# Kernel optimization log

Measured on AMD Instinct MI355X. Metric: run time of the kernel, lower is better.

## Reference

```python
import jax, jax.numpy as jnp
import numpy as np

N_WORDS, L_CHARS = 16384, 16
CHAR_SIZE, C_EMB = 128, 64
CONV_L, KERNEL, PAD = 256, 3, 2
VOCAB, D_EMB = 50000, 300
PAD_IDX = 1


def setup_inputs() -> dict:
    key = jax.random.key(0)
    k1, k2, k3, k4, k5, k6 = jax.random.split(key, 6)
    X = jax.random.randint(k1, (N_WORDS, L_CHARS), 0, CHAR_SIZE, dtype=jnp.int32)
    X_word = jax.random.randint(k2, (N_WORDS,), 0, VOCAB, dtype=jnp.int32)
    char_emb_w = jax.random.normal(k3, (CHAR_SIZE, C_EMB), dtype=jnp.float32)
    char_emb_w = char_emb_w.at[PAD_IDX].set(0.0)  # padding row zeroed, as in _init_char_embedding
    conv_w = jax.random.normal(k4, (CONV_L, C_EMB, KERNEL), dtype=jnp.float32) * 0.05
    conv_b = jax.random.normal(k5, (CONV_L,), dtype=jnp.float32) * 0.05
    word_emb_w = jax.random.normal(k6, (VOCAB, D_EMB), dtype=jnp.float32)
    return {"X": X, "X_word": X_word, "char_emb_w": char_emb_w,
            "conv_w": conv_w, "conv_b": conv_b, "word_emb_w": word_emb_w}


def reference(X, X_word, char_emb_w, conv_w, conv_b, word_emb_w):
    # char embedding lookup: [N, L, c_emb] -> NCH layout [N, c_emb, L]
    ce = char_emb_w[X].transpose(0, 2, 1)
    # Conv1d(c_emb -> conv_l, kernel=3, padding=2): out length L + 2*PAD - K + 1
    y = jax.lax.conv_general_dilated(
        ce, conv_w, window_strides=(1,), padding=[(PAD, PAD)],
        dimension_numbers=("NCH", "OIH", "NCH"))
    y = jax.nn.relu(y + conv_b[None, :, None])
    # MaxPool over the full time dimension -> [N, conv_l]
    char_feat = jnp.max(y, axis=2)
    # word embedding lookup: [N, d_emb]
    we = word_emb_w[X_word]
    return jnp.concatenate([char_feat, we], axis=1)
```

## Files before the change

### kernel.cpp

```cpp
#include <hip/hip_runtime.h>

#define N_WORDS   16384
#define L_CHARS   16
#define CHAR_SIZE 128
#define C_EMB     64
#define CONV_L    256
#define KERNEL_K  3
#define D_EMB     300
#define OUT_STRIDE (CONV_L + D_EMB)
#define CH_Q      64
#define SLICE_H   (CHAR_SIZE * KERNEL_K * CH_Q)

typedef _Float16 half8 __attribute__((ext_vector_type(8)));

static __device__ __forceinline__ half8 h8max(half8 a, half8 b) {
#if __has_builtin(__builtin_elementwise_max)
    return __builtin_elementwise_max(a, b);
#else
    half8 r;
    #pragma unroll
    for (int i = 0; i < 8; ++i) r[i] = a[i] > b[i] ? a[i] : b[i];
    return r;
#endif
}

__global__ void transpose_w(const float* __restrict__ w, float* __restrict__ Wt) {
    int tid = blockIdx.x * blockDim.x + threadIdx.x;
    if (tid >= CONV_L * C_EMB * KERNEL_K) return;
    int o = tid / (C_EMB * KERNEL_K);
    int r = tid - o * (C_EMB * KERNEL_K);
    int i = r / KERNEL_K;
    int k = r - i * KERNEL_K;
    Wt[i * (KERNEL_K * CONV_L) + k * CONV_L + o] = w[tid];
}

__global__ void build_table(const float* __restrict__ emb,
                            const float* __restrict__ Wt,
                            _Float16* __restrict__ Th) {
    int c = blockIdx.x / 3;
    int k = blockIdx.x % 3;
    int o = threadIdx.x;
    const float* erow = emb + c * C_EMB;
    float s = 0.f;
    #pragma unroll
    for (int i = 0; i < C_EMB; ++i)
        s += erow[i] * Wt[i * (KERNEL_K * CONV_L) + k * CONV_L + o];
    int q  = o >> 6;
    int oi = o & 63;
    Th[q * SLICE_H + c * (KERNEL_K * CH_Q) + k * CH_Q + oi] = (_Float16)s;
}

__global__ __launch_bounds__(256, 3)
void main_kernel(const int* __restrict__ X,
                 const int* __restrict__ Xw,
                 const _Float16* __restrict__ Th,
                 const float* __restrict__ conv_b,
                 const float* __restrict__ word_emb,
                 float* __restrict__ out,
                 int word_blocks) {
    __shared__ __align__(16) _Float16 Ts[SLICE_H];

    const int lane = threadIdx.x & 63;
    const int wv   = threadIdx.x >> 6;

    if ((int)blockIdx.x < word_blocks) {
        const int wavesTotal = word_blocks * 4;
        const int waveId = blockIdx.x * 4 + wv;
        for (int n = waveId; n < N_WORDS; n += wavesTotal) {
            int widx = Xw[n];
            const float4* src = (const float4*)(word_emb + (size_t)widx * D_EMB);
            float4* dst = (float4*)(out + (size_t)n * OUT_STRIDE + CONV_L);
            dst[lane] = src[lane];
            if (lane < (D_EMB / 4 - 64)) {
                dst[64 + lane] = src[64 + lane];
            }
        }
        return;
    }

    const int cb   = (int)blockIdx.x - word_blocks;
    const int q    = cb & 3;
    const int wgrp = cb >> 2;

    {
        const float4* src = (const float4*)(Th + q * SLICE_H);
        float4* dst = (float4*)Ts;
        #pragma unroll
        for (int i = 0; i < 12; ++i)
            dst[threadIdx.x + i * 256] = src[threadIdx.x + i * 256];
    }
    __syncthreads();

    const int g  = lane >> 3;
    const int l8 = lane & 7;

    float bias[8];
    {
        const float4* bp = (const float4*)(conv_b + q * CH_Q + l8 * 8);
        float4 b0 = bp[0], b1 = bp[1];
        bias[0]=b0.x; bias[1]=b0.y; bias[2]=b0.z; bias[3]=b0.w;
        bias[4]=b1.x; bias[5]=b1.y; bias[6]=b1.z; bias[7]=b1.w;
    }

    #pragma unroll
    for (int pass = 0; pass < 2; ++pass) {
        const int n = wgrp * 64 + pass * 32 + wv * 8 + g;

        const int4* xr = (const int4*)(X + n * L_CHARS);
        int4 q0 = xr[0], q1 = xr[1], q2 = xr[2], q3 = xr[3];
        int cs[16] = {q0.x, q0.y, q0.z, q0.w,
                      q1.x, q1.y, q1.z, q1.w,
                      q2.x, q2.y, q2.z, q2.w,
                      q3.x, q3.y, q3.z, q3.w};

        half8 a0 = (half8)(_Float16)0.f;
        half8 a1 = (half8)(_Float16)0.f;
        half8 m  = (half8)(_Float16)(-65504.f);

        #pragma unroll
        for (int j = 0; j < L_CHARS; ++j) {
            const _Float16* row = Ts + cs[j] * (KERNEL_K * CH_Q) + l8 * 8;
            half8 t0 = *(const half8*)(row);
            half8 t1 = *(const half8*)(row + CH_Q);
            half8 t2 = *(const half8*)(row + 2*CH_Q);
            half8 yj = a0 + t2;
            m  = h8max(m, yj);
            a0 = a1 + t1;
            a1 = t0;
        }
        m = h8max(m, a0);
        m = h8max(m, a1);

        float r[8];
        #pragma unroll
        for (int e = 0; e < 8; ++e)
            r[e] = fmaxf((float)m[e] + bias[e], 0.f);
        float4* dst = (float4*)(out + (size_t)n * OUT_STRIDE + q * CH_Q + l8 * 8);
        dst[0] = make_float4(r[0], r[1], r[2], r[3]);
        dst[1] = make_float4(r[4], r[5], r[6], r[7]);
    }
}

extern "C" void kernel_launch(void* const* d_in, const int* in_sizes, int n_in,
                              void* d_out, int out_size, void* d_ws, size_t ws_size,
                              hipStream_t stream) {
    const int*   X    = (const int*)d_in[0];
    const int*   Xw   = (const int*)d_in[1];
    const float* emb  = (const float*)d_in[2];
    const float* w    = (const float*)d_in[3];
    const float* b    = (const float*)d_in[4];
    const float* we   = (const float*)d_in[5];
    float* out = (float*)d_out;

    _Float16* Th = (_Float16*)d_ws;
    float*    Wt = (float*)((char*)d_ws + 4 * SLICE_H * sizeof(_Float16));

    transpose_w<<<(CONV_L * C_EMB * KERNEL_K + 255) / 256, 256, 0, stream>>>(w, Wt);
    build_table<<<CHAR_SIZE * KERNEL_K, 256, 0, stream>>>(emb, Wt, Th);

    const int WB = 256;
    const int CB = 1024;
    main_kernel<<<WB + CB, 256, 0, stream>>>(X, Xw, Th, b, we, out, WB);
}
```

Baseline: 134.4 us.

## Fuse weight transpose into table build and merge word gather into conv blocks

Drops the separate weight-transpose kernel: build_table now stages each 64-output chunk of conv weights in padded shared memory and computes all three taps per character block, which removes one launch. The main kernel shrinks from 1280 to 768 blocks. Each block processes one or two conv jobs in a grid-stride loop, and blocks 256 and up then gather 32 word-embedding rows each. Fewer launches and a grid that fits roughly one wave of residency are meant to cut launch and tail overhead. The cost is load imbalance, since some blocks do two conv jobs and others do a conv job plus word copies.

```diff
diff --git a/kernel.cpp b/kernel.cpp
--- a/kernel.cpp
+++ b/kernel.cpp
@@ -9,7 +9,8 @@
 #define D_EMB     300
 #define OUT_STRIDE (CONV_L + D_EMB)
 #define CH_Q      64
-#define SLICE_H   (CHAR_SIZE * KERNEL_K * CH_Q)
+#define T_ROWQ    (KERNEL_K * CH_Q)
+#define SLICE_H   (CHAR_SIZE * T_ROWQ)
 
 typedef _Float16 half8 __attribute__((ext_vector_type(8)));
 
@@ -24,30 +25,35 @@
 #endif
 }
 
-__global__ void transpose_w(const float* __restrict__ w, float* __restrict__ Wt) {
-    int tid = blockIdx.x * blockDim.x + threadIdx.x;
-    if (tid >= CONV_L * C_EMB * KERNEL_K) return;
-    int o = tid / (C_EMB * KERNEL_K);
-    int r = tid - o * (C_EMB * KERNEL_K);
-    int i = r / KERNEL_K;
-    int k = r - i * KERNEL_K;
-    Wt[i * (KERNEL_K * CONV_L) + k * CONV_L + o] = w[tid];
-}
+__global__ __launch_bounds__(256)
+void build_table(const float* __restrict__ emb,
+                 const float* __restrict__ w,
+                 _Float16* __restrict__ Th) {
+    __shared__ float wl[64 * 193];
+    const int c  = blockIdx.x;
+    const int t  = threadIdx.x;
+    const int kk = t >> 6;
+    const int ol = t & 63;
 
-__global__ void build_table(const float* __restrict__ emb,
-                            const float* __restrict__ Wt,
-                            _Float16* __restrict__ Th) {
-    int c = blockIdx.x / 3;
-    int k = blockIdx.x % 3;
-    int o = threadIdx.x;
-    const float* erow = emb + c * C_EMB;
-    float s = 0.f;
     #pragma unroll
-    for (int i = 0; i < C_EMB; ++i)
-        s += erow[i] * Wt[i * (KERNEL_K * CONV_L) + k * CONV_L + o];
-    int q  = o >> 6;
-    int oi = o & 63;
-    Th[q * SLICE_H + c * (KERNEL_K * CH_Q) + k * CH_Q + oi] = (_Float16)s;
+    for (int chunk = 0; chunk < 4; ++chunk) {
+        __syncthreads();
+        #pragma unroll
+        for (int j = 0; j < 48; ++j) {
+            int idx   = t + j * 256;
+            int o_loc = idx / 192;
+            int r     = idx - o_loc * 192;
+            wl[o_loc * 193 + r] = w[(size_t)(chunk * 64 + o_loc) * 192 + r];
+        }
+        __syncthreads();
+        if (kk < 3) {
+            float s = 0.f;
+            #pragma unroll
+            for (int i = 0; i < C_EMB; ++i)
+                s += emb[c * C_EMB + i] * wl[ol * 193 + i * 3 + kk];
+            Th[chunk * SLICE_H + c * T_ROWQ + kk * CH_Q + ol] = (_Float16)s;
+        }
+    }
 }
 
 __global__ __launch_bounds__(256, 3)
@@ -56,38 +62,21 @@
                  const _Float16* __restrict__ Th,
                  const float* __restrict__ conv_b,
                  const float* __restrict__ word_emb,
-                 float* __restrict__ out,
-                 int word_blocks) {
+                 float* __restrict__ out) {
     __shared__ __align__(16) _Float16 Ts[SLICE_H];
 
-    const int lane = threadIdx.x & 63;
-    const int wv   = threadIdx.x >> 6;
-
-    if ((int)blockIdx.x < word_blocks) {
-        const int wavesTotal = word_blocks * 4;
-        const int waveId = blockIdx.x * 4 + wv;
-        for (int n = waveId; n < N_WORDS; n += wavesTotal) {
-            int widx = Xw[n];
-            const float4* src = (const float4*)(word_emb + (size_t)widx * D_EMB);
-            float4* dst = (float4*)(out + (size_t)n * OUT_STRIDE + CONV_L);
-            dst[lane] = src[lane];
-            if (lane < (D_EMB / 4 - 64)) {
-                dst[64 + lane] = src[64 + lane];
-            }
-        }
-        return;
-    }
-
-    const int cb   = (int)blockIdx.x - word_blocks;
-    const int q    = cb & 3;
-    const int wgrp = cb >> 2;
+    const int b    = blockIdx.x;
+    const int t    = threadIdx.x;
+    const int lane = t & 63;
+    const int wv   = t >> 6;
+    const int q    = b & 3;
 
     {
         const float4* src = (const float4*)(Th + q * SLICE_H);
         float4* dst = (float4*)Ts;
         #pragma unroll
         for (int i = 0; i < 12; ++i)
-            dst[threadIdx.x + i * 256] = src[threadIdx.x + i * 256];
+            dst[t + i * 256] = src[t + i * 256];
     }
     __syncthreads();
 
@@ -102,42 +91,60 @@
         bias[4]=b1.x; bias[5]=b1.y; bias[6]=b1.z; bias[7]=b1.w;
     }
 
-    #pragma unroll
-    for (int pass = 0; pass < 2; ++pass) {
-        const int n = wgrp * 64 + pass * 32 + wv * 8 + g;
+    for (int job = b; job < 1024; job += 768) {
+        const int wgrp = job >> 2;
+        #pragma unroll
+        for (int pass = 0; pass < 2; ++pass) {
+            const int n = wgrp * 64 + pass * 32 + wv * 8 + g;
 
-        const int4* xr = (const int4*)(X + n * L_CHARS);
-        int4 q0 = xr[0], q1 = xr[1], q2 = xr[2], q3 = xr[3];
-        int cs[16] = {q0.x, q0.y, q0.z, q0.w,
-                      q1.x, q1.y, q1.z, q1.w,
-                      q2.x, q2.y, q2.z, q2.w,
-                      q3.x, q3.y, q3.z, q3.w};
+            const int4* xr = (const int4*)(X + n * L_CHARS);
+            int4 q0 = xr[0], q1 = xr[1], q2 = xr[2], q3 = xr[3];
+            int cs[16] = {q0.x, q0.y, q0.z, q0.w,
+                          q1.x, q1.y, q1.z, q1.w,
+                          q2.x, q2.y, q2.z, q2.w,
+                          q3.x, q3.y, q3.z, q3.w};
 
-        half8 a0 = (half8)(_Float16)0.f;
-        half8 a1 = (half8)(_Float16)0.f;
-        half8 m  = (half8)(_Float16)(-65504.f);
+            half8 a0 = (half8)(_Float16)0.f;
+            half8 a1 = (half8)(_Float16)0.f;
+            half8 m  = (half8)(_Float16)(-65504.f);
 
+            #pragma unroll
+            for (int j = 0; j < L_CHARS; ++j) {
+                const _Float16* row = Ts + cs[j] * T_ROWQ + l8 * 8;
+                half8 t0 = *(const half8*)(row);
+                half8 t1 = *(const half8*)(row + CH_Q);
+                half8 t2 = *(const half8*)(row + 2 * CH_Q);
+                half8 yj = a0 + t2;
+                m  = h8max(m, yj);
+                a0 = a1 + t1;
+                a1 = t0;
+            }
+            m = h8max(m, a0);
+            m = h8max(m, a1);
+
+            float r[8];
+            #pragma unroll
+            for (int e = 0; e < 8; ++e)
+                r[e] = fmaxf((float)m[e] + bias[e], 0.f);
+            float4* dst = (float4*)(out + (size_t)n * OUT_STRIDE + q * CH_Q + l8 * 8);
+            dst[0] = make_float4(r[0], r[1], r[2], r[3]);
+            dst[1] = make_float4(r[4], r[5], r[6], r[7]);
+        }
+    }
+
+    if (b >= 256) {
+        const int wb = b - 256;
         #pragma unroll
-        for (int j = 0; j < L_CHARS; ++j) {
-            const _Float16* row = Ts + cs[j] * (KERNEL_K * CH_Q) + l8 * 8;
-            half8 t0 = *(const half8*)(row);
-            half8 t1 = *(const half8*)(row + CH_Q);
-            half8 t2 = *(const half8*)(row + 2*CH_Q);
-            half8 yj = a0 + t2;
-            m  = h8max(m, yj);
-            a0 = a1 + t1;
-            a1 = t0;
+        for (int s = 0; s < 8; ++s) {
+            int n = wb * 32 + wv * 8 + s;
+            int widx = Xw[n];
+            const float4* src = (const float4*)(word_emb + (size_t)widx * D_EMB);
+            float4* dst = (float4*)(out + (size_t)n * OUT_STRIDE + CONV_L);
+            dst[lane] = src[lane];
+            if (lane < (D_EMB / 4 - 64)) {
+                dst[64 + lane] = src[64 + lane];
+            }
         }
-        m = h8max(m, a0);
-        m = h8max(m, a1);
-
-        float r[8];
-        #pragma unroll
-        for (int e = 0; e < 8; ++e)
-            r[e] = fmaxf((float)m[e] + bias[e], 0.f);
-        float4* dst = (float4*)(out + (size_t)n * OUT_STRIDE + q * CH_Q + l8 * 8);
-        dst[0] = make_float4(r[0], r[1], r[2], r[3]);
-        dst[1] = make_float4(r[4], r[5], r[6], r[7]);
     }
 }
 
@@ -153,12 +160,7 @@
     float* out = (float*)d_out;
 
     _Float16* Th = (_Float16*)d_ws;
-    float*    Wt = (float*)((char*)d_ws + 4 * SLICE_H * sizeof(_Float16));
 
-    transpose_w<<<(CONV_L * C_EMB * KERNEL_K + 255) / 256, 256, 0, stream>>>(w, Wt);
-    build_table<<<CHAR_SIZE * KERNEL_K, 256, 0, stream>>>(emb, Wt, Th);
-
-    const int WB = 256;
-    const int CB = 1024;
-    main_kernel<<<WB + CB, 256, 0, stream>>>(X, Xw, Th, b, we, out, WB);
+    build_table<<<CHAR_SIZE, 256, 0, stream>>>(emb, w, Th);
+    main_kernel<<<768, 256, 0, stream>>>(X, Xw, Th, b, we, out);
 }
```

Measured after the change: 165.6 us. +23.2%, slower.
